# Kernel optimization log

Measured on AMD Instinct MI355X. Metric: run time of the kernel, lower is better.

Reference implementation:

```python
import jax, jax.numpy as jnp
import numpy as np
import math

EMBED_DIM = 512
NUM_HEADS = 8
NUM_EXPERTS = 16
TOP_K = 8
B, T = 2, 1024


def setup_inputs() -> dict:
    key = jax.random.key(0)
    ks = jax.random.split(key, 16)
    d, E = EMBED_DIM, NUM_EXPERTS
    hdim = 4 * d  # expert hidden width
    s = 0.02
    inp = {
        "x": jax.random.normal(ks[0], (B, T, d), jnp.float32),
        # RMSNorm params (init ones, matching torch module)
        "g": jnp.ones((d,), jnp.float32),
        "b": jnp.ones((d,), jnp.float32),
        # attention
        "c_attn_w": jax.random.normal(ks[1], (d, 3 * d), jnp.float32) * s,
        "c_attn_b": jnp.zeros((3 * d,), jnp.float32),
        "alpha": jnp.ones((NUM_HEADS,), jnp.float32),
        "c_proj_w": jax.random.normal(ks[2], (d, d), jnp.float32) * s,
        "c_proj_b": jnp.zeros((d,), jnp.float32),
        # router
        "router_w": jax.random.normal(ks[3], (d, E), jnp.float32) * s,
        "router_b": jnp.zeros((E,), jnp.float32),
        # stacked expert params: Linear(d,4d) -> SwiGLU(4d,4d) -> Linear(4d,d)
        "w_in": jax.random.normal(ks[4], (E, d, hdim), jnp.float32) * s,
        "b_in": jnp.zeros((E, hdim), jnp.float32),
        "w1": jax.random.normal(ks[5], (E, hdim, 2 * hdim), jnp.float32) * s,
        "b1": jnp.zeros((E, 2 * hdim), jnp.float32),
        "w2": jax.random.normal(ks[6], (E, hdim, hdim), jnp.float32) * s,
        "b2": jnp.zeros((E, hdim), jnp.float32),
        "w_out": jax.random.normal(ks[7], (E, hdim, d), jnp.float32) * s,
        "b_out": jnp.zeros((E, d), jnp.float32),
    }
    return inp


def _block(x, g, b, c_attn_w, c_attn_b, alpha, c_proj_w, c_proj_b,
           router_w, router_b, w_in, b_in, w1, b1, w2, b2, w_out, b_out):
    Bb, Tt, C = x.shape
    H = alpha.shape[0]
    hd = C // H
    E = router_b.shape[0]

    # RMSNorm (note: additive b, per original module)
    rms = jnp.sqrt(jnp.mean(x * x, axis=-1, keepdims=True) + 1e-6)
    xn = (x / rms) * g + b

    # QK-normalized causal attention
    qkv = xn @ c_attn_w + c_attn_b                      # [B,T,3C]
    q, k, v = jnp.split(qkv, 3, axis=-1)
    def heads(t):
        return t.reshape(Bb, Tt, H, hd).transpose(0, 2, 1, 3)  # [B,H,T,hd]
    q, k, v = heads(q), heads(k), heads(v)
    eps = 1e-5
    q_hat = q / (jnp.linalg.norm(q, axis=-1, keepdims=True) + eps)
    k_hat = k / (jnp.linalg.norm(k, axis=-1, keepdims=True) + eps)
    factor = (alpha * math.sqrt(hd)).reshape(1, H, 1, 1)
    q_scaled = q_hat * factor
    # SDPA default scale = 1/sqrt(head_dim)
    scores = jnp.einsum("bhqd,bhkd->bhqk", q_scaled, k_hat) / math.sqrt(hd)
    causal = jnp.tril(jnp.ones((Tt, Tt), bool))
    scores = jnp.where(causal, scores, -jnp.inf)
    att = jax.nn.softmax(scores, axis=-1)
    y = jnp.einsum("bhqk,bhkd->bhqd", att, v)
    y = y.transpose(0, 2, 1, 3).reshape(Bb, Tt, C)
    y = y @ c_proj_w + c_proj_b
    x = x + y

    # Router + top-8 normalized gates
    routes = jax.nn.softmax(x @ router_w + router_b, axis=-1)  # [B,T,E]
    probs, idx = jax.lax.top_k(routes, TOP_K)
    probs = probs / jnp.sum(probs, axis=-1, keepdims=True)
    # combine weights per expert: [B,T,E]
    gates = jnp.sum(jax.nn.one_hot(idx, E, dtype=x.dtype) * probs[..., None], axis=2)

    # Dense expert evaluation (faithful math: unselected tokens get zero gate)
    N = Bb * Tt
    xf = x.reshape(N, C)
    gf = gates.reshape(N, E)
    h = jnp.einsum("nd,edf->enf", xf, w_in) + b_in[:, None, :]      # [E,N,4d]
    c = jnp.einsum("enf,efg->eng", h, w1) + b1[:, None, :]          # [E,N,8d]
    a, bb2 = jnp.split(c, 2, axis=-1)
    s = (bb2 * jax.nn.sigmoid(bb2)) * a                              # SwiGLU
    o = jnp.einsum("enf,efg->eng", s, w2) + b2[:, None, :]          # [E,N,4d]
    eo = jnp.einsum("enf,efd->end", o, w_out) + b_out[:, None, :]   # [E,N,d]
    moe = jnp.einsum("end,ne->nd", eo, gf).reshape(Bb, Tt, C)
    return x + moe


def reference(x, g, b, c_attn_w, c_attn_b, alpha, c_proj_w, c_proj_b,
              router_w, router_b, w_in, b_in, w1, b1, w2, b2, w_out, b_out):
    return _block(x, g, b, c_attn_w, c_attn_b, alpha, c_proj_w, c_proj_b,
                  router_w, router_b, w_in, b_in, w1, b1, w2, b2, w_out, b_out)
```

## Files before the change

kernel.cpp:

```cpp
#include <hip/hip_runtime.h>
#include <stdint.h>

#define DEVI __device__ __forceinline__

typedef short short8 __attribute__((ext_vector_type(8)));
typedef short short4v __attribute__((ext_vector_type(4)));
typedef float f32x4 __attribute__((ext_vector_type(4)));

DEVI float bf2f(unsigned short s){ union{unsigned u; float f;} x; x.u = ((unsigned)s)<<16; return x.f; }
DEVI unsigned short f2bf(float f){ union{float f; unsigned u;} x; x.f=f; unsigned r = x.u + 0x7fff + ((x.u>>16)&1); return (unsigned short)(r>>16); }

DEVI void gload_lds16(const void* g, void* l){
  __builtin_amdgcn_global_load_lds((const __attribute__((address_space(1))) unsigned int*)g,
                                   (__attribute__((address_space(3))) unsigned int*)l, 16, 0, 0);
}

__global__ __launch_bounds__(256)
void transpose_cvt(const float* __restrict__ in, unsigned short* __restrict__ out, int K, int N)
{
  __shared__ float tile[32][33];
  size_t zoff = (size_t)blockIdx.z * K * N;
  const float* src = in + zoff;
  unsigned short* dst = out + zoff;
  int kb = blockIdx.y*32, nb = blockIdx.x*32;
  int t = threadIdx.x;
  int tr = t>>3, tc = (t&7)*4;
  float4 v = *(const float4*)(src + (size_t)(kb+tr)*N + nb + tc);
  tile[tr][tc+0]=v.x; tile[tr][tc+1]=v.y; tile[tr][tc+2]=v.z; tile[tr][tc+3]=v.w;
  __syncthreads();
  short4v ov;
  ov[0] = (short)f2bf(tile[tc+0][tr]);
  ov[1] = (short)f2bf(tile[tc+1][tr]);
  ov[2] = (short)f2bf(tile[tc+2][tr]);
  ov[3] = (short)f2bf(tile[tc+3][tr]);
  *(short4v*)(dst + (size_t)(nb+tr)*K + kb + tc) = ov;
}

__global__ __launch_bounds__(256)
void rmsnorm_k(const float* __restrict__ x, const float* __restrict__ gw,
               const float* __restrict__ bw, unsigned short* __restrict__ xn)
{
  int row = blockIdx.x*4 + (threadIdx.x>>6);
  int lane = threadIdx.x & 63;
  const float* xr = x + (size_t)row*512 + lane*8;
  float4 a = *(const float4*)xr;
  float4 c = *(const float4*)(xr+4);
  float ss = a.x*a.x+a.y*a.y+a.z*a.z+a.w*a.w + c.x*c.x+c.y*c.y+c.z*c.z+c.w*c.w;
  #pragma unroll
  for (int m=1;m<64;m<<=1) ss += __shfl_xor(ss, m);
  float inv = 1.0f / sqrtf(ss*(1.f/512.f) + 1e-6f);
  const float* gr = gw + lane*8; const float* br = bw + lane*8;
  float4 g0=*(const float4*)gr, g1=*(const float4*)(gr+4);
  float4 b0=*(const float4*)br, b1=*(const float4*)(br+4);
  short8 o;
  o[0]=(short)f2bf(a.x*inv*g0.x + b0.x);
  o[1]=(short)f2bf(a.y*inv*g0.y + b0.y);
  o[2]=(short)f2bf(a.z*inv*g0.z + b0.z);
  o[3]=(short)f2bf(a.w*inv*g0.w + b0.w);
  o[4]=(short)f2bf(c.x*inv*g1.x + b1.x);
  o[5]=(short)f2bf(c.y*inv*g1.y + b1.y);
  o[6]=(short)f2bf(c.z*inv*g1.z + b1.z);
  o[7]=(short)f2bf(c.w*inv*g1.w + b1.w);
  *(short8*)(xn + (size_t)row*512 + lane*8) = o;
}

template<int EPI>
__global__ __launch_bounds__(256)
void gemm_bt(const unsigned short* __restrict__ A, const unsigned short* __restrict__ B,
             const float* __restrict__ bias,
             float* __restrict__ Cf, unsigned short* __restrict__ Ch,
             const float* __restrict__ resid, const unsigned short* __restrict__ aux,
             int M, int N, int K,
             const int* __restrict__ off, long long strideBz, long long strideBiasz)
{
  __shared__ char smem[32768];
  char* smA = smem; char* smB = smem + 16384;
  int z = blockIdx.z;
  int rowbase = 0, Mz = M;
  if (off){ rowbase = off[z]; Mz = off[z+1] - rowbase; }
  int row0 = blockIdx.y * 128;
  if (row0 >= Mz) return;
  int col0 = blockIdx.x * 128;
  const unsigned short* Bz = B + (size_t)z * strideBz;
  const float* biasz = bias + (size_t)z * strideBiasz;

  int t = threadIdx.x, w = t>>6, lane = t&63;
  int lrow = lane&15, lg = lane>>4;
  int wr = w>>1, wc = w&1;

  f32x4 acc[4][4];
  #pragma unroll
  for (int i=0;i<4;i++){
    #pragma unroll
    for (int j=0;j<4;j++) acc[i][j] = f32x4{0.f,0.f,0.f,0.f};
  }

  const size_t Abase = (size_t)(rowbase + row0) * K;
  const size_t Bbase = (size_t)col0 * K;

  int nkt = K >> 6;
  for (int kt=0; kt<nkt; kt++){
    __syncthreads();
    int k0 = kt*64;
    #pragma unroll
    for (int i=0;i<4;i++){
      int s = (i*4 + w)*64 + lane;
      int r = s>>3;
      int kb = (s&7) ^ (r&7);
      gload_lds16(A + Abase + (size_t)r*K + k0 + kb*8, smA + (size_t)(i*4+w)*1024);
      gload_lds16(Bz + Bbase + (size_t)r*K + k0 + kb*8, smB + (size_t)(i*4+w)*1024);
    }
    __syncthreads();
    #pragma unroll
    for (int ks=0; ks<2; ks++){
      short8 af[4], bf[4];
      int kbb = lg + ks*4;
      #pragma unroll
      for (int m=0;m<4;m++){
        int rt = wr*64 + m*16 + lrow;
        af[m] = *(const short8*)(smA + rt*128 + ((kbb ^ (rt&7))<<4));
      }
      #pragma unroll
      for (int n=0;n<4;n++){
        int rt = wc*64 + n*16 + lrow;
        bf[n] = *(const short8*)(smB + rt*128 + ((kbb ^ (rt&7))<<4));
      }
      #pragma unroll
      for (int m=0;m<4;m++){
        #pragma unroll
        for (int n=0;n<4;n++)
          acc[m][n] = __builtin_amdgcn_mfma_f32_16x16x32_bf16(af[m], bf[n], acc[m][n], 0,0,0);
      }
    }
  }

  #pragma unroll
  for (int m=0;m<4;m++){
    int rloc = wr*64 + m*16 + lg*4;
    #pragma unroll
    for (int j=0;j<4;j++){
      int row = row0 + rloc + j;
      if (row < Mz){
        size_t rg = (size_t)(rowbase + row);
        #pragma unroll
        for (int n=0;n<4;n++){
          int col = col0 + wc*64 + n*16 + lrow;
          float v = acc[m][n][j] + biasz[col];
          size_t idx = rg * N + col;
          if constexpr (EPI == 0){
            Cf[idx] = v;
          } else if constexpr (EPI == 1){
            Ch[idx] = f2bf(v);
          } else if constexpr (EPI == 2){
            float a = bf2f(aux[idx]);
            float sg = v / (1.f + __expf(-v));
            Ch[idx] = f2bf(a * sg);
          } else {
            v += resid[idx];
            Cf[idx] = v;
            Ch[idx] = f2bf(v);
          }
        }
      }
    }
  }
}

__global__ __launch_bounds__(256)
void prep_qkv(const float* __restrict__ qkv, const float* __restrict__ alpha,
              unsigned short* __restrict__ q_s, unsigned short* __restrict__ k_hat,
              unsigned short* __restrict__ v_t)
{
  int idx = blockIdx.x*4 + (threadIdx.x>>6);
  int lane = threadIdx.x & 63;
  int h = idx & 7, bt = idx >> 3;
  size_t base = (size_t)bt*1536 + h*64 + lane;
  float qv = qkv[base], kv = qkv[base+512], vv = qkv[base+1024];
  float qs2 = qv*qv, ks2 = kv*kv;
  #pragma unroll
  for (int m=1;m<64;m<<=1){ qs2 += __shfl_xor(qs2, m); ks2 += __shfl_xor(ks2, m); }
  float qh = qv / (sqrtf(qs2) + 1e-5f) * alpha[h];
  float kh = kv / (sqrtf(ks2) + 1e-5f);
  int b = bt >> 10, tt = bt & 1023;
  size_t hb = ((size_t)(b*8+h))*1024*64;
  q_s[hb + (size_t)tt*64 + lane] = f2bf(qh);
  k_hat[hb + (size_t)tt*64 + lane] = f2bf(kh);
  v_t[((size_t)(b*8+h)*64 + lane)*1024 + tt] = f2bf(vv);
}

__global__ __launch_bounds__(256)
void attn_k(const unsigned short* __restrict__ q_s, const unsigned short* __restrict__ k_hat,
            const unsigned short* __restrict__ v_t, unsigned short* __restrict__ y)
{
  __shared__ char sm[51200];
  char* smK = sm + 18432;
  char* smV = sm + 34816;
  int qt = blockIdx.x, bh = blockIdx.y;
  int b = bh>>3, h = bh&7;
  int t = threadIdx.x, w = t>>6, lane = t&63;
  int lrow = lane&15, lg = lane>>4;
  int q0 = qt*128;
  const size_t hQK = (size_t)bh*1024*64;
  const size_t hV  = (size_t)bh*64*1024;

  #pragma unroll
  for (int i=0;i<4;i++){
    int s = (i*4+w)*64 + lane;
    int r = s>>3, kb = (s&7)^(r&7);
    gload_lds16(q_s + hQK + (size_t)(q0+r)*64 + kb*8, sm + (size_t)(i*4+w)*1024);
  }
  __syncthreads();
  short8 qf[2][2];
  #pragma unroll
  for (int mf=0;mf<2;mf++){
    #pragma unroll
    for (int ks=0;ks<2;ks++){
      int rt = w*32 + mf*16 + lrow;
      int kbb = lg + ks*4;
      qf[mf][ks] = *(const short8*)(sm + rt*128 + ((kbb^(rt&7))<<4));
    }
  }
  f32x4 oacc[2][4];
  #pragma unroll
  for (int i=0;i<2;i++){
    #pragma unroll
    for (int j=0;j<4;j++) oacc[i][j] = f32x4{0.f,0.f,0.f,0.f};
  }
  float mrun[2][4], lrun[2][4];
  #pragma unroll
  for (int i=0;i<2;i++){
    #pragma unroll
    for (int j=0;j<4;j++){ mrun[i][j] = -1e30f; lrun[i][j] = 0.f; }
  }
  char* Pw = sm + w*4608;

  for (int kt=0; kt<=qt; kt++){
    __syncthreads();
    int t0 = kt*128;
    #pragma unroll
    for (int i=0;i<4;i++){
      int s = (i*4+w)*64 + lane;
      int r = s>>3, kb = (s&7)^(r&7);
      gload_lds16(k_hat + hQK + (size_t)(t0+r)*64 + kb*8, smK + (size_t)(i*4+w)*1024);
    }
    #pragma unroll
    for (int i=0;i<4;i++){
      int s = (i*4+w)*64 + lane;
      int d = s>>4, kb2 = s&15;
      int kb = kb2 ^ (d&7);
      gload_lds16(v_t + hV + (size_t)d*1024 + t0 + kb*8, smV + (size_t)(i*4+w)*1024);
    }
    __syncthreads();

    f32x4 sacc[2][8];
    #pragma unroll
    for (int i=0;i<2;i++){
      #pragma unroll
      for (int j=0;j<8;j++) sacc[i][j] = f32x4{0.f,0.f,0.f,0.f};
    }
    #pragma unroll
    for (int ks=0;ks<2;ks++){
      short8 kf[8];
      int kbb = lg + ks*4;
      #pragma unroll
      for (int nf=0;nf<8;nf++){
        int rt = nf*16+lrow;
        kf[nf] = *(const short8*)(smK + rt*128 + ((kbb^(rt&7))<<4));
      }
      #pragma unroll
      for (int mf=0;mf<2;mf++){
        #pragma unroll
        for (int nf=0;nf<8;nf++)
          sacc[mf][nf] = __builtin_amdgcn_mfma_f32_16x16x32_bf16(qf[mf][ks], kf[nf], sacc[mf][nf], 0,0,0);
      }
    }
    if (kt == qt){
      #pragma unroll
      for (int mf=0;mf<2;mf++){
        #pragma unroll
        for (int nf=0;nf<8;nf++){
          #pragma unroll
          for (int j=0;j<4;j++){
            int qi = w*32+mf*16+lg*4+j;
            int ki = nf*16 + lrow;
            if (ki > qi) sacc[mf][nf][j] = -1e30f;
          }
        }
      }
    }
    #pragma unroll
    for (int mf=0;mf<2;mf++){
      #pragma unroll
      for (int j=0;j<4;j++){
        float mx = sacc[mf][0][j];
        #pragma unroll
        for (int nf=1;nf<8;nf++) mx = fmaxf(mx, sacc[mf][nf][j]);
        #pragma unroll
        for (int m=1;m<16;m<<=1) mx = fmaxf(mx, __shfl_xor(mx, m));
        float mnew = fmaxf(mrun[mf][j], mx);
        float sc = __expf(mrun[mf][j] - mnew);
        float rs = 0.f;
        #pragma unroll
        for (int nf=0;nf<8;nf++){
          float p = __expf(sacc[mf][nf][j] - mnew);
          sacc[mf][nf][j] = p; rs += p;
        }
        #pragma unroll
        for (int m=1;m<16;m<<=1) rs += __shfl_xor(rs, m);
        lrun[mf][j] = lrun[mf][j]*sc + rs;
        mrun[mf][j] = mnew;
        #pragma unroll
        for (int n2=0;n2<4;n2++) oacc[mf][n2][j] *= sc;
      }
    }
    #pragma unroll
    for (int half=0; half<2; half++){
      #pragma unroll
      for (int mf=0;mf<2;mf++){
        #pragma unroll
        for (int nfh=0;nfh<4;nfh++){
          int nf = half*4 + nfh;
          #pragma unroll
          for (int j=0;j<4;j++){
            int row = mf*16 + lg*4 + j;
            int col = nfh*16 + lrow;
            *(unsigned short*)(Pw + (row*72 + col)*2) = f2bf(sacc[mf][nf][j]);
          }
        }
      }
      #pragma unroll
      for (int k2=0;k2<2;k2++){
        int ks2 = half*2 + k2;
        short8 pf[2], vf[4];
        #pragma unroll
        for (int mf=0;mf<2;mf++)
          pf[mf] = *(const short8*)(Pw + (mf*16+lrow)*144 + lg*16 + k2*64);
        #pragma unroll
        for (int n2=0;n2<4;n2++){
          int d = n2*16+lrow;
          int kbb2 = lg + ks2*4;
          vf[n2] = *(const short8*)(smV + d*256 + ((kbb2^(d&7))<<4));
        }
        #pragma unroll
        for (int mf=0;mf<2;mf++){
          #pragma unroll
          for (int n2=0;n2<4;n2++)
            oacc[mf][n2] = __builtin_amdgcn_mfma_f32_16x16x32_bf16(pf[mf], vf[n2], oacc[mf][n2], 0,0,0);
        }
      }
    }
  }
  #pragma unroll
  for (int mf=0;mf<2;mf++){
    #pragma unroll
    for (int n2=0;n2<4;n2++){
      #pragma unroll
      for (int j=0;j<4;j++){
        float v = oacc[mf][n2][j] / lrun[mf][j];
        int qi = q0 + w*32 + mf*16 + lg*4 + j;
        int d = n2*16 + lrow;
        y[((size_t)(b*1024+qi))*512 + h*64 + d] = f2bf(v);
      }
    }
  }
}

__global__ __launch_bounds__(256)
void router_topk(const float* __restrict__ x2f, const float* __restrict__ rw,
                 const float* __restrict__ rb, float* __restrict__ gates)
{
  int tkn = blockIdx.x*4 + (threadIdx.x>>6);
  int lane = threadIdx.x & 63;
  int e = lane & 15, p = lane >> 4;
  const float* xr = x2f + (size_t)tkn*512;
  float part = 0.f;
  for (int d = p*128; d < p*128+128; d++)
    part += xr[d] * rw[d*16 + e];
  part += __shfl_xor(part, 16);
  part += __shfl_xor(part, 32);
  float logit = part + rb[e];
  float mx = logit;
  #pragma unroll
  for (int m=1;m<16;m<<=1) mx = fmaxf(mx, __shfl_xor(mx, m));
  float ex = __expf(logit - mx);
  float sm = ex;
  #pragma unroll
  for (int m=1;m<16;m<<=1) sm += __shfl_xor(sm, m);
  float prob = ex / sm;
  bool taken = false;
  float ssum = 0.f;
  #pragma unroll
  for (int r=0;r<8;r++){
    float cv = taken ? -1.f : prob;
    int ci = e;
    #pragma unroll
    for (int m=1;m<16;m<<=1){
      float ov = __shfl_xor(cv, m);
      int oi = __shfl_xor(ci, m);
      if (ov > cv || (ov == cv && oi < ci)){ cv = ov; ci = oi; }
    }
    if (e == ci) taken = true;
    ssum += cv;
  }
  if (lane < 16)
    gates[(size_t)tkn*16 + e] = taken ? prob / ssum : 0.f;
}

__global__ void listbuild(const float* __restrict__ gates, int* __restrict__ list,
                          int* __restrict__ slot, int* __restrict__ cnt)
{
  int e = blockIdx.x;
  int tid = threadIdx.x, w = tid>>6, lane = tid&63;
  __shared__ int sbase;
  __shared__ int wsum[4];
  if (tid==0) sbase = 0;
  __syncthreads();
  for (int c=0;c<8;c++){
    int tk = c*256 + tid;
    bool flag = gates[(size_t)tk*16 + e] > 0.f;
    unsigned long long bal = __ballot(flag);
    if (lane==0) wsum[w] = (int)__popcll(bal);
    __syncthreads();
    int wpref = 0;
    for (int i=0;i<w;i++) wpref += wsum[i];
    int tot = wsum[0]+wsum[1]+wsum[2]+wsum[3];
    int lpref = (int)__popcll(bal & ((1ull<<lane)-1ull));
    if (flag){
      int pos = sbase + wpref + lpref;
      list[e*2048 + pos] = tk;
      slot[(size_t)tk*16 + e] = pos;
    }
    __syncthreads();
    if (tid==0) sbase += tot;
    __syncthreads();
  }
  if (tid==0) cnt[e] = sbase;
}

__global__ void prefix_off(const int* __restrict__ cnt, int* __restrict__ off){
  if (threadIdx.x==0 && blockIdx.x==0){
    int a=0;
    for (int e=0;e<16;e++){ off[e]=a; a+=cnt[e]; }
    off[16]=a;
  }
}

__global__ __launch_bounds__(256)
void gather_rows(const unsigned short* __restrict__ x2h, const int* __restrict__ list,
                 const int* __restrict__ cnt, const int* __restrict__ off,
                 unsigned short* __restrict__ xe)
{
  int e = blockIdx.y;
  int s = blockIdx.x*4 + (threadIdx.x>>6);
  if (s >= cnt[e]) return;
  int lane = threadIdx.x & 63;
  int tk = list[e*2048 + s];
  *(short8*)(xe + ((size_t)(off[e]+s))*512 + lane*8) =
      *(const short8*)(x2h + (size_t)tk*512 + lane*8);
}

__global__ __launch_bounds__(256)
void combine_k(const float* __restrict__ x2f, const unsigned short* __restrict__ eo,
               const float* __restrict__ gates, const int* __restrict__ slot,
               const int* __restrict__ off, float* __restrict__ out)
{
  int tkn = blockIdx.x;
  __shared__ float gs[16];
  __shared__ int rws[16];
  int tid = threadIdx.x;
  if (tid < 16){
    float g = gates[(size_t)tkn*16 + tid];
    gs[tid] = g;
    rws[tid] = (g > 0.f) ? (off[tid] + slot[(size_t)tkn*16 + tid]) : 0;
  }
  __syncthreads();
  for (int d = tid; d < 512; d += 256){
    float v = x2f[(size_t)tkn*512 + d];
    #pragma unroll
    for (int e=0;e<16;e++){
      float g = gs[e];
      if (g > 0.f) v += g * bf2f(eo[(size_t)rws[e]*512 + d]);
    }
    out[(size_t)tkn*512 + d] = v;
  }
}

extern "C" void kernel_launch(void* const* d_in, const int* in_sizes, int n_in,
                              void* d_out, int out_size, void* d_ws, size_t ws_size,
                              hipStream_t stream) {
  (void)in_sizes; (void)n_in; (void)out_size; (void)ws_size;
  const float* x    = (const float*)d_in[0];
  const float* gw   = (const float*)d_in[1];
  const float* bw   = (const float*)d_in[2];
  const float* caw  = (const float*)d_in[3];
  const float* cab  = (const float*)d_in[4];
  const float* alpha= (const float*)d_in[5];
  const float* cpw  = (const float*)d_in[6];
  const float* cpb  = (const float*)d_in[7];
  const float* rw   = (const float*)d_in[8];
  const float* rb   = (const float*)d_in[9];
  const float* w_in = (const float*)d_in[10];
  const float* b_in = (const float*)d_in[11];
  const float* w1   = (const float*)d_in[12];
  const float* b1   = (const float*)d_in[13];
  const float* w2   = (const float*)d_in[14];
  const float* b2   = (const float*)d_in[15];
  const float* w_out= (const float*)d_in[16];
  const float* b_out= (const float*)d_in[17];

  char* ws = (char*)d_ws;
  size_t o = 0;
  auto alloc = [&](size_t bytes)->char*{
    char* p = ws + o;
    o += (bytes + 255) & ~(size_t)255;
    return p;
  };
  unsigned short* wT_attn = (unsigned short*)alloc(1536ull*512*2);
  unsigned short* wT_proj = (unsigned short*)alloc(512ull*512*2);
  unsigned short* wT_in   = (unsigned short*)alloc(16ull*2048*512*2);
  unsigned short* wT_1    = (unsigned short*)alloc(16ull*4096*2048*2);
  unsigned short* wT_2    = (unsigned short*)alloc(16ull*2048*2048*2);
  unsigned short* wT_out  = (unsigned short*)alloc(16ull*512*2048*2);
  unsigned short* xn      = (unsigned short*)alloc(2048ull*512*2);
  float*          qkv     = (float*)alloc(2048ull*1536*4);
  unsigned short* q_s     = (unsigned short*)alloc(2048ull*512*2);
  unsigned short* k_hat   = (unsigned short*)alloc(2048ull*512*2);
  unsigned short* v_t     = (unsigned short*)alloc(2048ull*512*2);
  unsigned short* ybuf    = (unsigned short*)alloc(2048ull*512*2);
  float*          x2f     = (float*)alloc(2048ull*512*4);
  unsigned short* x2h     = (unsigned short*)alloc(2048ull*512*2);
  float*          gates   = (float*)alloc(2048ull*16*4);
  int*            slot    = (int*)alloc(2048ull*16*4);
  int*            list    = (int*)alloc(16ull*2048*4);
  int*            cnt     = (int*)alloc(64);
  int*            off     = (int*)alloc(256);
  unsigned short* xe      = (unsigned short*)alloc(16512ull*512*2);
  unsigned short* hbuf    = (unsigned short*)alloc(16512ull*2048*2);
  unsigned short* c1buf   = (unsigned short*)alloc(16512ull*2048*2);
  unsigned short* sbuf    = (unsigned short*)alloc(16512ull*2048*2);
  unsigned short* eobuf   = xe;
  unsigned short* obuf    = hbuf;

  dim3 blk(256);
  transpose_cvt<<<dim3(1536/32, 512/32, 1), blk, 0, stream>>>(caw, wT_attn, 512, 1536);
  transpose_cvt<<<dim3(512/32, 512/32, 1), blk, 0, stream>>>(cpw, wT_proj, 512, 512);
  transpose_cvt<<<dim3(2048/32, 512/32, 16), blk, 0, stream>>>(w_in, wT_in, 512, 2048);
  transpose_cvt<<<dim3(4096/32, 2048/32, 16), blk, 0, stream>>>(w1, wT_1, 2048, 4096);
  transpose_cvt<<<dim3(2048/32, 2048/32, 16), blk, 0, stream>>>(w2, wT_2, 2048, 2048);
  transpose_cvt<<<dim3(512/32, 2048/32, 16), blk, 0, stream>>>(w_out, wT_out, 2048, 512);

  rmsnorm_k<<<512, blk, 0, stream>>>(x, gw, bw, xn);
  gemm_bt<0><<<dim3(12,16,1), blk, 0, stream>>>(xn, wT_attn, cab, qkv, nullptr, nullptr, nullptr,
                                                2048, 1536, 512, nullptr, 0, 0);
  prep_qkv<<<4096, blk, 0, stream>>>(qkv, alpha, q_s, k_hat, v_t);
  attn_k<<<dim3(8,16), blk, 0, stream>>>(q_s, k_hat, v_t, ybuf);
  gemm_bt<3><<<dim3(4,16,1), blk, 0, stream>>>(ybuf, wT_proj, cpb, x2f, x2h, x, nullptr,
                                               2048, 512, 512, nullptr, 0, 0);
  router_topk<<<512, blk, 0, stream>>>(x2f, rw, rb, gates);
  listbuild<<<16, blk, 0, stream>>>(gates, list, slot, cnt);
  prefix_off<<<1, 64, 0, stream>>>(cnt, off);
  gather_rows<<<dim3(512,16), blk, 0, stream>>>(x2h, list, cnt, off, xe);

  gemm_bt<1><<<dim3(16,16,16), blk, 0, stream>>>(xe, wT_in, b_in, nullptr, hbuf, nullptr, nullptr,
                                                 0, 2048, 512, off, 2048ll*512, 2048);
  gemm_bt<1><<<dim3(16,16,16), blk, 0, stream>>>(hbuf, wT_1, b1, nullptr, c1buf, nullptr, nullptr,
                                                 0, 2048, 2048, off, 4096ll*2048, 4096);
  gemm_bt<2><<<dim3(16,16,16), blk, 0, stream>>>(hbuf, wT_1 + 2048ull*2048, b1 + 2048, nullptr, sbuf,
                                                 nullptr, c1buf, 0, 2048, 2048, off, 4096ll*2048, 4096);
  gemm_bt<1><<<dim3(16,16,16), blk, 0, stream>>>(sbuf, wT_2, b2, nullptr, obuf, nullptr, nullptr,
                                                 0, 2048, 2048, off, 2048ll*2048, 2048);
  gemm_bt<1><<<dim3(4,16,16), blk, 0, stream>>>(obuf, wT_out, b_out, nullptr, eobuf, nullptr, nullptr,
                                                0, 512, 2048, off, 512ll*2048, 512);
  combine_k<<<2048, blk, 0, stream>>>(x2f, eobuf, gates, slot, off, (float*)d_out);
}
```

Before: 1.249 ms.

## Replace expert GEMMs with 256x128-tile triple-buffered pipelined kernel

```diff
diff --git a/kernel.cpp b/kernel.cpp
--- a/kernel.cpp
+++ b/kernel.cpp
@@ -2,6 +2,7 @@
 #include <stdint.h>
 
 #define DEVI __device__ __forceinline__
+#define FENCE() asm volatile("" ::: "memory")
 
 typedef short short8 __attribute__((ext_vector_type(8)));
 typedef short short4v __attribute__((ext_vector_type(4)));
@@ -65,28 +66,29 @@
 }
 
 template<int EPI>
-__global__ __launch_bounds__(256)
-void gemm_bt(const unsigned short* __restrict__ A, const unsigned short* __restrict__ B,
-             const float* __restrict__ bias,
-             float* __restrict__ Cf, unsigned short* __restrict__ Ch,
-             const float* __restrict__ resid, const unsigned short* __restrict__ aux,
-             int M, int N, int K,
-             const int* __restrict__ off, long long strideBz, long long strideBiasz)
-{
-  __shared__ char smem[32768];
-  char* smA = smem; char* smB = smem + 16384;
+__global__ __launch_bounds__(512, 2)
+void gemm3(const unsigned short* __restrict__ A, const unsigned short* __restrict__ B,
+           const float* __restrict__ bias,
+           float* __restrict__ Cf, unsigned short* __restrict__ Ch,
+           const unsigned short* __restrict__ aux,
+           int M, int N, int K,
+           const int* __restrict__ off, long long strideBz, long long strideBiasz)
+{
+  __shared__ char smem[147456];
   int z = blockIdx.z;
   int rowbase = 0, Mz = M;
   if (off){ rowbase = off[z]; Mz = off[z+1] - rowbase; }
-  int row0 = blockIdx.y * 128;
+  int row0 = blockIdx.y * 256;
   if (row0 >= Mz) return;
   int col0 = blockIdx.x * 128;
-  const unsigned short* Bz = B + (size_t)z * strideBz;
+  const unsigned short* Ab = A + (size_t)(rowbase + row0) * K;
+  const unsigned short* Bb = B + (size_t)z * strideBz + (size_t)col0 * K;
   const float* biasz = bias + (size_t)z * strideBiasz;
 
-  int t = threadIdx.x, w = t>>6, lane = t&63;
-  int lrow = lane&15, lg = lane>>4;
-  int wr = w>>1, wc = w&1;
+  int tid = threadIdx.x;
+  int lane = tid & 63, w = tid >> 6;
+  int lrow = lane & 15, lg = lane >> 4;
+  int wr = w >> 1, wc = w & 1;
 
   f32x4 acc[4][4];
   #pragma unroll
@@ -95,43 +97,91 @@
     for (int j=0;j<4;j++) acc[i][j] = f32x4{0.f,0.f,0.f,0.f};
   }
 
-  const size_t Abase = (size_t)(rowbase + row0) * K;
-  const size_t Bbase = (size_t)col0 * K;
-
   int nkt = K >> 6;
-  for (int kt=0; kt<nkt; kt++){
-    __syncthreads();
-    int k0 = kt*64;
-    #pragma unroll
-    for (int i=0;i<4;i++){
-      int s = (i*4 + w)*64 + lane;
-      int r = s>>3;
-      int kb = (s&7) ^ (r&7);
-      gload_lds16(A + Abase + (size_t)r*K + k0 + kb*8, smA + (size_t)(i*4+w)*1024);
-      gload_lds16(Bz + Bbase + (size_t)r*K + k0 + kb*8, smB + (size_t)(i*4+w)*1024);
-    }
-    __syncthreads();
-    #pragma unroll
-    for (int ks=0; ks<2; ks++){
-      short8 af[4], bf[4];
-      int kbb = lg + ks*4;
-      #pragma unroll
-      for (int m=0;m<4;m++){
-        int rt = wr*64 + m*16 + lrow;
-        af[m] = *(const short8*)(smA + rt*128 + ((kbb ^ (rt&7))<<4));
-      }
+
+  auto stage = [&](int kt2, int part){
+    if (kt2 >= nkt) return;
+    char* sA = smem + (kt2 % 3) * 49152;
+    char* sB = sA + 32768;
+    int k0 = kt2 << 6;
+    #pragma unroll
+    for (int i=0;i<2;i++){
+      int s = (part*2 + i)*512 + tid;
+      int r = s >> 3, kb = (s & 7) ^ (r & 7);
+      gload_lds16(Ab + (size_t)r*K + k0 + kb*8, sA + s*16);
+    }
+    {
+      int s = part*512 + tid;
+      int r = s >> 3, kb = (s & 7) ^ (r & 7);
+      gload_lds16(Bb + (size_t)r*K + k0 + kb*8, sB + s*16);
+    }
+  };
+
+  stage(0,0); stage(0,1); stage(1,0); stage(1,1);
+  asm volatile("s_waitcnt vmcnt(6)" ::: "memory");
+  __builtin_amdgcn_s_barrier();
+  FENCE();
+
+  for (int kt = 0; kt < nkt; kt++){
+    char* sA = smem + (kt % 3) * 49152;
+    char* sB = sA + 32768;
+    short8 bfr[4][2], afr[4][2];
+    #pragma unroll
+    for (int n=0;n<4;n++){
+      int ct = wc*64 + n*16 + lrow;
+      #pragma unroll
+      for (int kk=0;kk<2;kk++){
+        int kbb = lg + kk*4;
+        bfr[n][kk] = *(const short8*)(sB + ct*128 + ((kbb ^ (ct&7))<<4));
+      }
+    }
+    #pragma unroll
+    for (int m=0;m<2;m++){
+      int rt = wr*64 + m*16 + lrow;
+      #pragma unroll
+      for (int kk=0;kk<2;kk++){
+        int kbb = lg + kk*4;
+        afr[m][kk] = *(const short8*)(sA + rt*128 + ((kbb ^ (rt&7))<<4));
+      }
+    }
+    stage(kt+2, 0);
+    FENCE(); __builtin_amdgcn_s_barrier(); FENCE();
+    __builtin_amdgcn_s_setprio(1);
+    #pragma unroll
+    for (int m=0;m<2;m++){
       #pragma unroll
       for (int n=0;n<4;n++){
-        int rt = wc*64 + n*16 + lrow;
-        bf[n] = *(const short8*)(smB + rt*128 + ((kbb ^ (rt&7))<<4));
-      }
-      #pragma unroll
-      for (int m=0;m<4;m++){
-        #pragma unroll
-        for (int n=0;n<4;n++)
-          acc[m][n] = __builtin_amdgcn_mfma_f32_16x16x32_bf16(af[m], bf[n], acc[m][n], 0,0,0);
-      }
-    }
+        #pragma unroll
+        for (int kk=0;kk<2;kk++)
+          acc[m][n] = __builtin_amdgcn_mfma_f32_16x16x32_bf16(afr[m][kk], bfr[n][kk], acc[m][n], 0,0,0);
+      }
+    }
+    __builtin_amdgcn_s_setprio(0);
+    FENCE(); __builtin_amdgcn_s_barrier(); FENCE();
+    #pragma unroll
+    for (int m=2;m<4;m++){
+      int rt = wr*64 + m*16 + lrow;
+      #pragma unroll
+      for (int kk=0;kk<2;kk++){
+        int kbb = lg + kk*4;
+        afr[m][kk] = *(const short8*)(sA + rt*128 + ((kbb ^ (rt&7))<<4));
+      }
+    }
+    stage(kt+2, 1);
+    FENCE(); __builtin_amdgcn_s_barrier(); FENCE();
+    __builtin_amdgcn_s_setprio(1);
+    #pragma unroll
+    for (int m=2;m<4;m++){
+      #pragma unroll
+      for (int n=0;n<4;n++){
+        #pragma unroll
+        for (int kk=0;kk<2;kk++)
+          acc[m][n] = __builtin_amdgcn_mfma_f32_16x16x32_bf16(afr[m][kk], bfr[n][kk], acc[m][n], 0,0,0);
+      }
+    }
+    __builtin_amdgcn_s_setprio(0);
+    asm volatile("s_waitcnt vmcnt(6)" ::: "memory");
+    FENCE(); __builtin_amdgcn_s_barrier(); FENCE();
   }
 
   #pragma unroll
@@ -151,16 +201,89 @@
             Cf[idx] = v;
           } else if constexpr (EPI == 1){
             Ch[idx] = f2bf(v);
-          } else if constexpr (EPI == 2){
+          } else {
             float a = bf2f(aux[idx]);
             float sg = v / (1.f + __expf(-v));
             Ch[idx] = f2bf(a * sg);
-          } else {
-            v += resid[idx];
-            Cf[idx] = v;
-            Ch[idx] = f2bf(v);
           }
         }
+      }
+    }
+  }
+}
+
+__global__ __launch_bounds__(256)
+void gemm_proj(const unsigned short* __restrict__ A, const unsigned short* __restrict__ B,
+               const float* __restrict__ bias,
+               float* __restrict__ Cf, unsigned short* __restrict__ Ch,
+               const float* __restrict__ resid, int M, int N, int K)
+{
+  __shared__ char smem[32768];
+  char* smA = smem; char* smB = smem + 16384;
+  int row0 = blockIdx.y * 128;
+  int col0 = blockIdx.x * 128;
+  int t = threadIdx.x, w = t>>6, lane = t&63;
+  int lrow = lane&15, lg = lane>>4;
+  int wr = w>>1, wc = w&1;
+
+  f32x4 acc[4][4];
+  #pragma unroll
+  for (int i=0;i<4;i++){
+    #pragma unroll
+    for (int j=0;j<4;j++) acc[i][j] = f32x4{0.f,0.f,0.f,0.f};
+  }
+  const size_t Abase = (size_t)row0 * K;
+  const size_t Bbase = (size_t)col0 * K;
+  int nkt = K >> 6;
+  for (int kt=0; kt<nkt; kt++){
+    __syncthreads();
+    int k0 = kt*64;
+    #pragma unroll
+    for (int i=0;i<4;i++){
+      int s = (i*4 + w)*64 + lane;
+      int r = s>>3;
+      int kb = (s&7) ^ (r&7);
+      gload_lds16(A + Abase + (size_t)r*K + k0 + kb*8, smA + (size_t)(i*4+w)*1024);
+      gload_lds16(B + Bbase + (size_t)r*K + k0 + kb*8, smB + (size_t)(i*4+w)*1024);
+    }
+    __syncthreads();
+    #pragma unroll
+    for (int ks=0; ks<2; ks++){
+      short8 af[4], bf[4];
+      int kbb = lg + ks*4;
+      #pragma unroll
+      for (int m=0;m<4;m++){
+        int rt = wr*64 + m*16 + lrow;
+        af[m] = *(const short8*)(smA + rt*128 + ((kbb ^ (rt&7))<<4));
+      }
+      #pragma unroll
+      for (int n=0;n<4;n++){
+        int rt = wc*64 + n*16 + lrow;
+        bf[n] = *(const short8*)(smB + rt*128 + ((kbb ^ (rt&7))<<4));
+      }
+      #pragma unroll
+      for (int m=0;m<4;m++){
+        #pragma unroll
+        for (int n=0;n<4;n++)
+          acc[m][n] = __builtin_amdgcn_mfma_f32_16x16x32_bf16(af[m], bf[n], acc[m][n], 0,0,0);
+      }
+    }
+  }
+  #pragma unroll
+  for (int m=0;m<4;m++){
+    int rloc = wr*64 + m*16 + lg*4;
+    #pragma unroll
+    for (int j=0;j<4;j++){
+      int row = row0 + rloc + j;
+      size_t rg = (size_t)row;
+      #pragma unroll
+      for (int n=0;n<4;n++){
+        int col = col0 + wc*64 + n*16 + lrow;
+        float v = acc[m][n][j] + bias[col];
+        size_t idx = rg * N + col;
+        v += resid[idx];
+        Cf[idx] = v;
+        Ch[idx] = f2bf(v);
       }
     }
   }
@@ -515,6 +638,7 @@
     o += (bytes + 255) & ~(size_t)255;
     return p;
   };
+  const size_t PADROWS = 16896;
   unsigned short* wT_attn = (unsigned short*)alloc(1536ull*512*2);
   unsigned short* wT_proj = (unsigned short*)alloc(512ull*512*2);
   unsigned short* wT_in   = (unsigned short*)alloc(16ull*2048*512*2);
@@ -534,14 +658,15 @@
   int*            list    = (int*)alloc(16ull*2048*4);
   int*            cnt     = (int*)alloc(64);
   int*            off     = (int*)alloc(256);
-  unsigned short* xe      = (unsigned short*)alloc(16512ull*512*2);
-  unsigned short* hbuf    = (unsigned short*)alloc(16512ull*2048*2);
-  unsigned short* c1buf   = (unsigned short*)alloc(16512ull*2048*2);
-  unsigned short* sbuf    = (unsigned short*)alloc(16512ull*2048*2);
+  unsigned short* xe      = (unsigned short*)alloc(PADROWS*512*2);
+  unsigned short* hbuf    = (unsigned short*)alloc(PADROWS*2048*2);
+  unsigned short* c1buf   = (unsigned short*)alloc(PADROWS*2048*2);
+  unsigned short* sbuf    = (unsigned short*)alloc(PADROWS*2048*2);
   unsigned short* eobuf   = xe;
   unsigned short* obuf    = hbuf;
 
   dim3 blk(256);
+  dim3 blk5(512);
   transpose_cvt<<<dim3(1536/32, 512/32, 1), blk, 0, stream>>>(caw, wT_attn, 512, 1536);
   transpose_cvt<<<dim3(512/32, 512/32, 1), blk, 0, stream>>>(cpw, wT_proj, 512, 512);
   transpose_cvt<<<dim3(2048/32, 512/32, 16), blk, 0, stream>>>(w_in, wT_in, 512, 2048);
@@ -550,26 +675,25 @@
   transpose_cvt<<<dim3(512/32, 2048/32, 16), blk, 0, stream>>>(w_out, wT_out, 2048, 512);
 
   rmsnorm_k<<<512, blk, 0, stream>>>(x, gw, bw, xn);
-  gemm_bt<0><<<dim3(12,16,1), blk, 0, stream>>>(xn, wT_attn, cab, qkv, nullptr, nullptr, nullptr,
+  gemm3<0><<<dim3(12, 8, 1), blk5, 0, stream>>>(xn, wT_attn, cab, qkv, nullptr, nullptr,
                                                 2048, 1536, 512, nullptr, 0, 0);
   prep_qkv<<<4096, blk, 0, stream>>>(qkv, alpha, q_s, k_hat, v_t);
   attn_k<<<dim3(8,16), blk, 0, stream>>>(q_s, k_hat, v_t, ybuf);
-  gemm_bt<3><<<dim3(4,16,1), blk, 0, stream>>>(ybuf, wT_proj, cpb, x2f, x2h, x, nullptr,
-                                               2048, 512, 512, nullptr, 0, 0);
+  gemm_proj<<<dim3(4,16,1), blk, 0, stream>>>(ybuf, wT_proj, cpb, x2f, x2h, x, 2048, 512, 512);
   router_topk<<<512, blk, 0, stream>>>(x2f, rw, rb, gates);
   listbuild<<<16, blk, 0, stream>>>(gates, list, slot, cnt);
   prefix_off<<<1, 64, 0, stream>>>(cnt, off);
   gather_rows<<<dim3(512,16), blk, 0, stream>>>(x2h, list, cnt, off, xe);
 
-  gemm_bt<1><<<dim3(16,16,16), blk, 0, stream>>>(xe, wT_in, b_in, nullptr, hbuf, nullptr, nullptr,
-                                                 0, 2048, 512, off, 2048ll*512, 2048);
-  gemm_bt<1><<<dim3(16,16,16), blk, 0, stream>>>(hbuf, wT_1, b1, nullptr, c1buf, nullptr, nullptr,
-                                                 0, 2048, 2048, off, 4096ll*2048, 4096);
-  gemm_bt<2><<<dim3(16,16,16), blk, 0, stream>>>(hbuf, wT_1 + 2048ull*2048, b1 + 2048, nullptr, sbuf,
-                                                 nullptr, c1buf, 0, 2048, 2048, off, 4096ll*2048, 4096);
-  gemm_bt<1><<<dim3(16,16,16), blk, 0, stream>>>(sbuf, wT_2, b2, nullptr, obuf, nullptr, nullptr,
-                                                 0, 2048, 2048, off, 2048ll*2048, 2048);
-  gemm_bt<1><<<dim3(4,16,16), blk, 0, stream>>>(obuf, wT_out, b_out, nullptr, eobuf, nullptr, nullptr,
-                                                0, 512, 2048, off, 512ll*2048, 512);
+  gemm3<1><<<dim3(16,8,16), blk5, 0, stream>>>(xe, wT_in, b_in, nullptr, hbuf, nullptr,
+                                               0, 2048, 512, off, 2048ll*512, 2048);
+  gemm3<1><<<dim3(16,8,16), blk5, 0, stream>>>(hbuf, wT_1, b1, nullptr, c1buf, nullptr,
+                                               0, 2048, 2048, off, 4096ll*2048, 4096);
+  gemm3<2><<<dim3(16,8,16), blk5, 0, stream>>>(hbuf, wT_1 + 2048ull*2048, b1 + 2048, nullptr, sbuf,
+                                               c1buf, 0, 2048, 2048, off, 4096ll*2048, 4096);
+  gemm3<1><<<dim3(16,8,16), blk5, 0, stream>>>(sbuf, wT_2, b2, nullptr, obuf, nullptr,
+                                               0, 2048, 2048, off, 2048ll*2048, 2048);
+  gemm3<1><<<dim3(4,8,16), blk5, 0, stream>>>(obuf, wT_out, b_out, nullptr, eobuf, nullptr,
+                                              0, 512, 2048, off, 512ll*2048, 512);
   combine_k<<<2048, blk, 0, stream>>>(x2f, eobuf, gates, slot, off, (float*)d_out);
 }
```

Measured after the change: 1.173 ms. 6.1% less time.
